# Optimization experiments

Measured on AMD Instinct MI355X. Metric: run time of the kernel, lower is better.

## Reference

```python
import jax, jax.numpy as jnp
import numpy as np
import math

B, C, D, NH, L, DFF = 128, 112, 512, 8, 13, 1920
DK = D // NH  # 64
_pos = np.arange(64)
_ranks, _files = _pos // 8, _pos % 8
RIDX = np.clip(_ranks[:, None] - _ranks[None, :], -7, 7) + 7  # [64,64] rel-rank bucket
FIDX = np.clip(_files[:, None] - _files[None, :], -7, 7) + 7  # [64,64] rel-file bucket
DIAG = _ranks + _files        # [64] in [0,14]
ADIAG = _ranks - _files + 7   # [64] in [0,14]


def _ln(x, g, b):
    m = jnp.mean(x, -1, keepdims=True)
    v = jnp.mean((x - m) ** 2, -1, keepdims=True)
    return (x - m) * jax.lax.rsqrt(v + 1e-5) * g + b


def setup_inputs() -> dict:
    key = jax.random.key(0)
    ks = iter(jax.random.split(key, 40))
    nrm = lambda *s: jax.random.normal(next(ks), s, jnp.float32) * 0.02
    return dict(
        x=jax.random.normal(next(ks), (B, C, 8, 8), jnp.float32),
        conv_w=nrm(C, D), conv_b=jnp.zeros(D),
        cls_token=nrm(1, 1, D),
        abs_pos=nrm(1, 64, D),
        file_emb=nrm(8, D), rank_emb=nrm(8, D),
        diag_emb=nrm(15, D), anti_diag_emb=nrm(15, D),
        ln1_g=jnp.ones((L, D)), ln1_b=jnp.zeros((L, D)),
        wq=nrm(L, D, D), bq=jnp.zeros((L, D)),
        wk=nrm(L, D, D), bk=jnp.zeros((L, D)),
        wv=nrm(L, D, D), bv=jnp.zeros((L, D)),
        wo=nrm(L, D, D), bo=jnp.zeros((L, D)),
        rel_bias=nrm(L, 15, 15, NH),
        ln2_g=jnp.ones((L, D)), ln2_b=jnp.zeros((L, D)),
        w_ff1=nrm(L, D, 2 * DFF), b_ff1=jnp.zeros((L, 2 * DFF)),
        w_ff2=nrm(L, DFF, D), b_ff2=jnp.zeros((L, D)),
        out_g=jnp.ones(D), out_b=jnp.zeros(D),
        vw1=nrm(D, D // 2), vb1=jnp.zeros(D // 2),
        vw2=nrm(D // 2, 128), vb2=jnp.zeros(128),
        vw3=nrm(128, 3), vb3=jnp.zeros(3),
        pw=nrm(D, 72), pb=jnp.zeros(72),
    )


def reference(x, conv_w, conv_b, cls_token, abs_pos, file_emb, rank_emb, diag_emb, anti_diag_emb,
              ln1_g, ln1_b, wq, bq, wk, bk, wv, bv, wo, bo, rel_bias, ln2_g, ln2_b,
              w_ff1, b_ff1, w_ff2, b_ff2, out_g, out_b,
              vw1, vb1, vw2, vb2, vw3, vb3, pw, pb):
    Bc = x.shape[0]
    # 1x1 conv == channel-wise linear; flatten spatial (row-major: s = rank*8 + file)
    tok = jnp.einsum('bcs,cd->bsd', x.reshape(Bc, C, 64), conv_w) + conv_b  # [B,64,D]
    pos = abs_pos + file_emb[_files] + rank_emb[_ranks] + diag_emb[DIAG] + anti_diag_emb[ADIAG]
    tok = tok + pos
    h = jnp.concatenate([jnp.broadcast_to(cls_token, (Bc, 1, D)), tok], axis=1)  # [B,65,D]
    scale = 1.0 / math.sqrt(DK)

    def block(hx, p):
        g1, b1, Wq, Bq, Wk, Bk, Wv, Bv, Wo, Bo, rb, g2, b2, W1, B1, W2, B2 = p
        n = _ln(hx, g1, b1)
        q = (n @ Wq + Bq).reshape(Bc, 65, NH, DK).transpose(0, 2, 1, 3)
        k = (n @ Wk + Bk).reshape(Bc, 65, NH, DK).transpose(0, 2, 1, 3)
        v = (n @ Wv + Bv).reshape(Bc, 65, NH, DK).transpose(0, 2, 1, 3)
        # gather relative-position bias [64,64,H] -> [H,65,65] with zero row/col for CLS
        bias = jnp.pad(jnp.transpose(rb[RIDX, FIDX], (2, 0, 1)), ((0, 0), (1, 0), (1, 0)))
        scores = jnp.einsum('bhqd,bhkd->bhqk', q, k) * scale + bias[None]
        a = jax.nn.softmax(scores, axis=-1)
        ctx = jnp.einsum('bhqk,bhkd->bhqd', a, v).transpose(0, 2, 1, 3).reshape(Bc, 65, D)
        hx = hx + ctx @ Wo + Bo
        n2 = _ln(hx, g2, b2)
        u = n2 @ W1 + B1
        u1, u2 = jnp.split(u, 2, axis=-1)
        hx = hx + (jax.nn.gelu(u1, approximate=False) * u2) @ W2 + B2
        return hx, None

    params = (ln1_g, ln1_b, wq, bq, wk, bk, wv, bv, wo, bo, rel_bias,
              ln2_g, ln2_b, w_ff1, b_ff1, w_ff2, b_ff2)
    h, _ = jax.lax.scan(block, h, params)
    h = _ln(h, out_g, out_b)
    cls = h[:, 0]
    v1 = jax.nn.gelu(cls @ vw1 + vb1, approximate=False)
    v2 = jax.nn.gelu(v1 @ vw2 + vb2, approximate=False)
    value = v2 @ vw3 + vb3                 # WDL logits [B,3]
    policy = (h[:, 1:] @ pw + pb).reshape(Bc, -1)  # [B, 64*72]
    return policy, value
```

## Files before the change

### kernel.cpp

```cpp
#include <hip/hip_runtime.h>
#include <stdint.h>

#define NLAYER 13
#define DMODEL 512
#define SEQ    65
#define BATCH  128
#define MROWS  (BATCH*SEQ)
#define NHEAD  8
#define DFFH   1920
#define MTILES 65
#define MBAND  9

typedef __bf16 bf16x8 __attribute__((ext_vector_type(8)));
typedef float  f32x4  __attribute__((ext_vector_type(4)));

__device__ __forceinline__ float bf2f(unsigned short u) {
    union { unsigned int i; float f; } c; c.i = ((unsigned int)u) << 16; return c.f;
}
__device__ __forceinline__ unsigned short f2bf(float f) {
    union { float f; unsigned int i; } c; c.f = f;
    unsigned int u = c.i;
    u += 0x7fffu + ((u >> 16) & 1u);
    return (unsigned short)(u >> 16);
}
__device__ __forceinline__ float gelu_exact(float x) {
    return 0.5f * x * (1.0f + erff(x * 0.70710678118654752f));
}

__global__ __launch_bounds__(256) void transpose_f32_bf16(
    const float* __restrict__ src, unsigned short* __restrict__ dst,
    int R, int C, int Cpad, long srcLS, long dstLS, int rowOff)
{
    __shared__ float tile[32][33];
    int l  = blockIdx.z;
    int c0 = blockIdx.x * 32, r0 = blockIdx.y * 32;
    const float* s = src + (long)l * srcLS;
    unsigned short* d = dst + (long)l * dstLS;
    int tx = threadIdx.x, ty = threadIdx.y;
#pragma unroll
    for (int k = 0; k < 4; k++) {
        int r = r0 + ty + 8*k, c = c0 + tx;
        float v = (r < R && c < C) ? s[(long)r * C + c] : 0.0f;
        tile[ty + 8*k][tx] = v;
    }
    __syncthreads();
#pragma unroll
    for (int k = 0; k < 4; k++) {
        int c = c0 + ty + 8*k, r = r0 + tx;
        if (c < Cpad && r < R)
            d[(long)(rowOff + c) * R + r] = f2bf(tile[tx][ty + 8*k]);
    }
}

__global__ __launch_bounds__(256) void stack_bias_kernel(
    const float* __restrict__ bq, const float* __restrict__ bk,
    const float* __restrict__ bv, float* __restrict__ bqkv)
{
    int idx = blockIdx.x * 256 + threadIdx.x;
    if (idx >= NLAYER * 1536) return;
    int l = idx / 1536, r = idx - l * 1536;
    float v;
    if (r < 512)       v = bq[l*512 + r];
    else if (r < 1024) v = bk[l*512 + r - 512];
    else               v = bv[l*512 + r - 1024];
    bqkv[idx] = v;
}

__global__ __launch_bounds__(256) void embed_kernel(
    const float* __restrict__ x, const float* __restrict__ conv_w,
    const float* __restrict__ conv_b, const float* __restrict__ cls_tok,
    const float* __restrict__ abs_pos, const float* __restrict__ file_emb,
    const float* __restrict__ rank_emb, const float* __restrict__ diag_emb,
    const float* __restrict__ adiag_emb, float* __restrict__ h)
{
    int b = blockIdx.y, sg = blockIdx.x, t = threadIdx.x;
    if (sg == 8) {
        for (int d = t; d < 512; d += 256)
            h[(long)b * SEQ * 512 + d] = cls_tok[d];
        return;
    }
    __shared__ float xs[112][8];
    for (int idx = t; idx < 112*8; idx += 256) {
        int c = idx >> 3, j = idx & 7;
        xs[c][j] = x[((long)b*112 + c)*64 + sg*8 + j];
    }
    __syncthreads();
    int d0 = t, d1 = t + 256;
    float acc0[8] = {}, acc1[8] = {};
    for (int c = 0; c < 112; c++) {
        float w0 = conv_w[c*512 + d0], w1 = conv_w[c*512 + d1];
#pragma unroll
        for (int j = 0; j < 8; j++) { acc0[j] += xs[c][j]*w0; acc1[j] += xs[c][j]*w1; }
    }
#pragma unroll
    for (int j = 0; j < 8; j++) {
        int sq = sg*8 + j, r = sq >> 3, f = sq & 7;
        long row = ((long)b * SEQ + 1 + sq) * 512;
        h[row + d0] = acc0[j] + conv_b[d0] + abs_pos[sq*512+d0] + file_emb[f*512+d0]
                    + rank_emb[r*512+d0] + diag_emb[(r+f)*512+d0] + adiag_emb[(r-f+7)*512+d0];
        h[row + d1] = acc1[j] + conv_b[d1] + abs_pos[sq*512+d1] + file_emb[f*512+d1]
                    + rank_emb[r*512+d1] + diag_emb[(r+f)*512+d1] + adiag_emb[(r-f+7)*512+d1];
    }
}

__global__ __launch_bounds__(256) void ln_kernel(
    const float* __restrict__ hx, const float* __restrict__ g,
    const float* __restrict__ bb, unsigned short* __restrict__ o)
{
    int row  = blockIdx.x * 4 + (threadIdx.x >> 6);
    int lane = threadIdx.x & 63;
    const float4* xr = (const float4*)(hx + (long)row * 512);
    float4 v0 = xr[lane], v1 = xr[lane + 64];
    float s  = v0.x+v0.y+v0.z+v0.w + v1.x+v1.y+v1.z+v1.w;
    float s2 = v0.x*v0.x+v0.y*v0.y+v0.z*v0.z+v0.w*v0.w
             + v1.x*v1.x+v1.y*v1.y+v1.z*v1.z+v1.w*v1.w;
    for (int off = 32; off; off >>= 1) { s += __shfl_xor(s, off); s2 += __shfl_xor(s2, off); }
    float mean = s * (1.0f/512.0f);
    float var  = s2 * (1.0f/512.0f) - mean*mean;
    float rs   = rsqrtf(var + 1e-5f);
    const float4* gr = (const float4*)g; const float4* br = (const float4*)bb;
    float4 g0 = gr[lane], g1 = gr[lane+64], b0 = br[lane], b1 = br[lane+64];
    ushort4 o0, o1;
    o0.x = f2bf((v0.x-mean)*rs*g0.x + b0.x);
    o0.y = f2bf((v0.y-mean)*rs*g0.y + b0.y);
    o0.z = f2bf((v0.z-mean)*rs*g0.z + b0.z);
    o0.w = f2bf((v0.w-mean)*rs*g0.w + b0.w);
    o1.x = f2bf((v1.x-mean)*rs*g1.x + b1.x);
    o1.y = f2bf((v1.y-mean)*rs*g1.y + b1.y);
    o1.z = f2bf((v1.z-mean)*rs*g1.z + b1.z);
    o1.w = f2bf((v1.w-mean)*rs*g1.w + b1.w);
    ushort4* orow = (ushort4*)(o + (long)row * 512);
    orow[lane] = o0; orow[lane + 64] = o1;
}

template<int MODE>
__global__ __launch_bounds__(256) void gemm128(
    const unsigned short* __restrict__ A, const unsigned short* __restrict__ Bt,
    const float* __restrict__ bias, const float* __restrict__ res,
    void* __restrict__ out, int K, int ldo, int nT)
{
    __shared__ __attribute__((aligned(16))) unsigned short As[128*32];
    __shared__ __attribute__((aligned(16))) unsigned short Bs[128*32];
    int id = blockIdx.x;
    int xcd = id & 7, jj = id >> 3;
    int bn  = jj % nT;
    int mt  = xcd * MBAND + jj / nT;
    if (mt >= MTILES) return;
    int m0 = mt * 128;
    int tid = threadIdx.x;
    int lane = tid & 63, w = tid >> 6;
    int quad = lane >> 4, col = lane & 15;

    int srow = tid >> 2;
    int sc8  = (tid & 3) * 8;

    int br0, br1;
    if (MODE == 2) {
        br0 = bn*64 + srow;
        br1 = 1920 + bn*64 + srow;
    } else {
        br0 = bn*128 + srow;
        br1 = bn*128 + srow + 64;
    }
    const unsigned short* Arow0 = A + (long)(m0 + srow) * K + sc8;
    const unsigned short* Arow1 = A + (long)(m0 + srow + 64) * K + sc8;
    const unsigned short* Brow0 = Bt + (long)br0 * K + sc8;
    const unsigned short* Brow1 = Bt + (long)br1 * K + sc8;

    f32x4 acc[2][8] = {};

    int4 ca0 = *(const int4*)(Arow0);
    int4 ca1 = *(const int4*)(Arow1);
    int4 cb0 = *(const int4*)(Brow0);
    int4 cb1 = *(const int4*)(Brow1);

    for (int k0 = 0; k0 < K; k0 += 32) {
        __syncthreads();
        *(int4*)(&As[srow*32 + sc8])        = ca0;
        *(int4*)(&As[(srow+64)*32 + sc8])   = ca1;
        *(int4*)(&Bs[srow*32 + sc8])        = cb0;
        *(int4*)(&Bs[(srow+64)*32 + sc8])   = cb1;
        __syncthreads();
        int kn = k0 + 32;
        if (kn < K) {
            ca0 = *(const int4*)(Arow0 + kn);
            ca1 = *(const int4*)(Arow1 + kn);
            cb0 = *(const int4*)(Brow0 + kn);
            cb1 = *(const int4*)(Brow1 + kn);
        }
        bf16x8 af[2], bfr[8];
#pragma unroll
        for (int i = 0; i < 2; i++)
            af[i] = *(const bf16x8*)(&As[(w*32 + i*16 + col)*32 + quad*8]);
#pragma unroll
        for (int t = 0; t < 8; t++)
            bfr[t] = *(const bf16x8*)(&Bs[(t*16 + col)*32 + quad*8]);
#pragma unroll
        for (int i = 0; i < 2; i++)
#pragma unroll
            for (int t = 0; t < 8; t++)
                acc[i][t] = __builtin_amdgcn_mfma_f32_16x16x32_bf16(af[i], bfr[t], acc[i][t], 0, 0, 0);
    }

    if (MODE == 2) {
        unsigned short* O = (unsigned short*)out;
        int gn0 = bn * 64;
#pragma unroll
        for (int i = 0; i < 2; i++)
#pragma unroll
        for (int t = 0; t < 4; t++) {
            int c = t*16 + col;
            float b1v = bias[gn0 + c];
            float b2v = bias[1920 + gn0 + c];
#pragma unroll
            for (int r = 0; r < 4; r++) {
                int m = m0 + w*32 + i*16 + quad*4 + r;
                float u1 = acc[i][t][r]   + b1v;
                float u2 = acc[i][t+4][r] + b2v;
                O[(long)m * DFFH + gn0 + c] = f2bf(gelu_exact(u1) * u2);
            }
        }
        return;
    }
    int n0 = bn * 128;
#pragma unroll
    for (int i = 0; i < 2; i++)
#pragma unroll
    for (int t = 0; t < 8; t++) {
        int cg = n0 + t*16 + col;
        float bv = (MODE == 3) ? (cg < 72 ? bias[cg] : 0.0f) : bias[cg];
#pragma unroll
        for (int r = 0; r < 4; r++) {
            int m = m0 + w*32 + i*16 + quad*4 + r;
            float v = acc[i][t][r] + bv;
            if (MODE == 0) {
                ((unsigned short*)out)[(long)m * ldo + cg] = f2bf(v);
            } else if (MODE == 1) {
                ((float*)out)[(long)m * ldo + cg] = res[(long)m * ldo + cg] + v;
            } else {
                if (cg < 72) {
                    int b2 = m / 65, s = m - b2 * 65;
                    if (s > 0)
                        ((float*)out)[(long)b2 * 4608 + (s - 1) * 72 + cg] = v;
                }
            }
        }
    }
}

__global__ __launch_bounds__(256) void attn_mfma_kernel(
    const unsigned short* __restrict__ qkv,
    const float* __restrict__ rel_bias,
    unsigned short* __restrict__ ctx,
    int layer)
{
    constexpr int QS = 72;
    constexpr int VS = 104;
    constexpr int SS = 68;
    constexpr int PS = 104;
    __shared__ __attribute__((aligned(16))) unsigned short Qs[80*QS];
    __shared__ __attribute__((aligned(16))) unsigned short Ks[80*QS];
    __shared__ __attribute__((aligned(16))) unsigned short Vt[64*VS];
    __shared__ __attribute__((aligned(16))) float Sf[65*SS];
    __shared__ __attribute__((aligned(16))) unsigned short Pb[80*PS];
    __shared__ float bias_s[225];

    int h = blockIdx.x, b = blockIdx.y, t = threadIdx.x;
    int lane = t & 63, w = t >> 6;
    int quad = lane >> 4, col = lane & 15;

    for (int i = t; i < 225; i += 256)
        bias_s[i] = rel_bias[((long)layer*225 + i)*8 + h];

    for (int i = t; i < 65*8; i += 256) {
        int s = i >> 3, c8 = (i & 7) * 8;
        const unsigned short* row = qkv + ((long)(b*65+s))*1536 + h*64 + c8;
        int4 qv = *(const int4*)(row);
        int4 kv = *(const int4*)(row + 512);
        int4 vv = *(const int4*)(row + 1024);
        unsigned short qsc[8];
        const unsigned short* qp = (const unsigned short*)&qv;
#pragma unroll
        for (int j = 0; j < 8; j++) qsc[j] = f2bf(bf2f(qp[j]) * 0.125f);
        *(int4*)&Qs[s*QS + c8] = *(const int4*)qsc;
        *(int4*)&Ks[s*QS + c8] = kv;
        const unsigned short* vp = (const unsigned short*)&vv;
#pragma unroll
        for (int j = 0; j < 8; j++) Vt[(c8+j)*VS + s] = vp[j];
    }
    for (int i = t; i < 64*31; i += 256) {
        int d = i / 31, s = 65 + i % 31;
        Vt[d*VS + s] = 0;
    }
    __syncthreads();

    for (int tt = w; tt < 25; tt += 4) {
        int mi = tt / 5, nj = tt % 5;
        f32x4 acc = {};
        bf16x8 a0 = *(const bf16x8*)&Qs[(mi*16+col)*QS + quad*8];
        bf16x8 b0 = *(const bf16x8*)&Ks[(nj*16+col)*QS + quad*8];
        acc = __builtin_amdgcn_mfma_f32_16x16x32_bf16(a0, b0, acc, 0, 0, 0);
        bf16x8 a1 = *(const bf16x8*)&Qs[(mi*16+col)*QS + 32 + quad*8];
        bf16x8 b1 = *(const bf16x8*)&Ks[(nj*16+col)*QS + 32 + quad*8];
        acc = __builtin_amdgcn_mfma_f32_16x16x32_bf16(a1, b1, acc, 0, 0, 0);
#pragma unroll
        for (int r = 0; r < 4; r++) {
            int qi = mi*16 + quad*4 + r, kj = nj*16 + col;
            if (qi < 65 && kj < 65) {
                float v = acc[r];
                if (qi >= 1 && kj >= 1) {
                    int i2 = qi - 1, j2 = kj - 1;
                    int dr = (i2 >> 3) - (j2 >> 3) + 7;
                    int df = (i2 & 7) - (j2 & 7) + 7;
                    v += bias_s[dr*15 + df];
                }
                Sf[qi*SS + kj] = v;
            }
        }
    }
    __syncthreads();

    for (int r = w; r < 65; r += 4) {
        float x0 = Sf[r*SS + lane];
        float x1 = (lane == 0) ? Sf[r*SS + 64] : -1e30f;
        float mx = fmaxf(x0, x1);
        for (int off = 32; off; off >>= 1) mx = fmaxf(mx, __shfl_xor(mx, off));
        float e0 = __expf(x0 - mx);
        float e1 = (lane == 0) ? __expf(x1 - mx) : 0.0f;
        float sm = e0 + e1;
        for (int off = 32; off; off >>= 1) sm += __shfl_xor(sm, off);
        float inv = 1.0f / sm;
        Pb[r*PS + lane] = f2bf(e0 * inv);
        if (lane == 0)  Pb[r*PS + 64] = f2bf(e1 * inv);
        if (lane >= 1 && lane <= 31) Pb[r*PS + 64 + lane] = 0;
    }
    __syncthreads();

    for (int tt = w; tt < 20; tt += 4) {
        int mi = tt >> 2, dj = tt & 3;
        f32x4 acc = {};
#pragma unroll
        for (int ks = 0; ks < 3; ks++) {
            bf16x8 a  = *(const bf16x8*)&Pb[(mi*16+col)*PS + ks*32 + quad*8];
            bf16x8 bb = *(const bf16x8*)&Vt[(dj*16+col)*VS + ks*32 + quad*8];
            acc = __builtin_amdgcn_mfma_f32_16x16x32_bf16(a, bb, acc, 0, 0, 0);
        }
#pragma unroll
        for (int r = 0; r < 4; r++) {
            int qi = mi*16 + quad*4 + r;
            if (qi < 65)
                ctx[((long)(b*65+qi))*512 + h*64 + dj*16 + col] = f2bf(acc[r]);
        }
    }
}

__global__ __launch_bounds__(256) void value_head_kernel(
    const unsigned short* __restrict__ hn,
    const float* __restrict__ vw1, const float* __restrict__ vb1,
    const float* __restrict__ vw2, const float* __restrict__ vb2,
    const float* __restrict__ vw3, const float* __restrict__ vb3,
    float* __restrict__ outv)
{
    int b = blockIdx.x, t = threadIdx.x;
    __shared__ float cls[512], v1[256], v2[128];
    for (int d = t; d < 512; d += 256) cls[d] = bf2f(hn[(long)b * SEQ * 512 + d]);
    __syncthreads();
    {
        float a = vb1[t];
        for (int c = 0; c < 512; c++) a += cls[c] * vw1[c*256 + t];
        v1[t] = gelu_exact(a);
    }
    __syncthreads();
    if (t < 128) {
        float a = vb2[t];
        for (int c = 0; c < 256; c++) a += v1[c] * vw2[c*128 + t];
        v2[t] = gelu_exact(a);
    }
    __syncthreads();
    if (t < 3) {
        float a = vb3[t];
        for (int c = 0; c < 128; c++) a += v2[c] * vw3[c*3 + t];
        outv[b*3 + t] = a;
    }
}

extern "C" void kernel_launch(void* const* d_in, const int* in_sizes, int n_in,
                              void* d_out, int out_size, void* d_ws, size_t ws_size,
                              hipStream_t stream)
{
    (void)in_sizes; (void)n_in; (void)out_size; (void)ws_size;
    const float* x        = (const float*)d_in[0];
    const float* conv_w   = (const float*)d_in[1];
    const float* conv_b   = (const float*)d_in[2];
    const float* cls_tok  = (const float*)d_in[3];
    const float* abs_pos  = (const float*)d_in[4];
    const float* file_emb = (const float*)d_in[5];
    const float* rank_emb = (const float*)d_in[6];
    const float* diag_emb = (const float*)d_in[7];
    const float* adiag    = (const float*)d_in[8];
    const float* ln1_g    = (const float*)d_in[9];
    const float* ln1_b    = (const float*)d_in[10];
    const float* wq       = (const float*)d_in[11];
    const float* bq       = (const float*)d_in[12];
    const float* wk       = (const float*)d_in[13];
    const float* bk       = (const float*)d_in[14];
    const float* wv       = (const float*)d_in[15];
    const float* bv       = (const float*)d_in[16];
    const float* wo       = (const float*)d_in[17];
    const float* bo       = (const float*)d_in[18];
    const float* rel_bias = (const float*)d_in[19];
    const float* ln2_g    = (const float*)d_in[20];
    const float* ln2_b    = (const float*)d_in[21];
    const float* w_ff1    = (const float*)d_in[22];
    const float* b_ff1    = (const float*)d_in[23];
    const float* w_ff2    = (const float*)d_in[24];
    const float* b_ff2    = (const float*)d_in[25];
    const float* out_g    = (const float*)d_in[26];
    const float* out_b    = (const float*)d_in[27];
    const float* vw1      = (const float*)d_in[28];
    const float* vb1      = (const float*)d_in[29];
    const float* vw2      = (const float*)d_in[30];
    const float* vb2      = (const float*)d_in[31];
    const float* vw3      = (const float*)d_in[32];
    const float* vb3      = (const float*)d_in[33];
    const float* pw       = (const float*)d_in[34];
    const float* pb       = (const float*)d_in[35];

    char* p = (char*)d_ws;
    auto alloc = [&](size_t bytes) { void* r = (void*)p; p += (bytes + 255) & ~(size_t)255; return r; };
    unsigned short* qkvT = (unsigned short*)alloc((size_t)NLAYER*1536*512*2);
    unsigned short* woT  = (unsigned short*)alloc((size_t)NLAYER*512*512*2);
    unsigned short* w1T  = (unsigned short*)alloc((size_t)NLAYER*3840*512*2);
    unsigned short* w2T  = (unsigned short*)alloc((size_t)NLAYER*512*1920*2);
    unsigned short* pwT  = (unsigned short*)alloc((size_t)128*512*2);
    float*          bqkv = (float*)alloc((size_t)NLAYER*1536*4);
    float*          h    = (float*)alloc((size_t)MROWS*512*4);
    unsigned short* nbf  = (unsigned short*)alloc((size_t)MROWS*512*2);
    unsigned short* qkvb = (unsigned short*)alloc((size_t)MROWS*1536*2);
    unsigned short* ctxb = (unsigned short*)alloc((size_t)MROWS*512*2);
    unsigned short* gbuf = (unsigned short*)alloc((size_t)MROWS*1920*2);

    dim3 tb(32, 8);
    transpose_f32_bf16<<<dim3(16,16,NLAYER), tb, 0, stream>>>(wq, qkvT, 512, 512, 512, 512L*512, 1536L*512, 0);
    transpose_f32_bf16<<<dim3(16,16,NLAYER), tb, 0, stream>>>(wk, qkvT, 512, 512, 512, 512L*512, 1536L*512, 512);
    transpose_f32_bf16<<<dim3(16,16,NLAYER), tb, 0, stream>>>(wv, qkvT, 512, 512, 512, 512L*512, 1536L*512, 1024);
    transpose_f32_bf16<<<dim3(16,16,NLAYER), tb, 0, stream>>>(wo, woT, 512, 512, 512, 512L*512, 512L*512, 0);
    transpose_f32_bf16<<<dim3(120,16,NLAYER), tb, 0, stream>>>(w_ff1, w1T, 512, 3840, 3840, 512L*3840, 3840L*512, 0);
    transpose_f32_bf16<<<dim3(16,60,NLAYER), tb, 0, stream>>>(w_ff2, w2T, 1920, 512, 512, 1920L*512, 512L*1920, 0);
    transpose_f32_bf16<<<dim3(4,16,1), tb, 0, stream>>>(pw, pwT, 512, 72, 128, 0, 0, 0);
    stack_bias_kernel<<<(NLAYER*1536 + 255)/256, 256, 0, stream>>>(bq, bk, bv, bqkv);

    embed_kernel<<<dim3(9, BATCH), 256, 0, stream>>>(x, conv_w, conv_b, cls_tok, abs_pos,
                                                     file_emb, rank_emb, diag_emb, adiag, h);

    for (int l = 0; l < NLAYER; l++) {
        ln_kernel<<<MROWS/4, 256, 0, stream>>>(h, ln1_g + l*512, ln1_b + l*512, nbf);
        gemm128<0><<<72*12, 256, 0, stream>>>(nbf, qkvT + (size_t)l*1536*512,
                                              bqkv + l*1536, nullptr, qkvb, 512, 1536, 12);
        attn_mfma_kernel<<<dim3(NHEAD, BATCH), 256, 0, stream>>>(qkvb, rel_bias, ctxb, l);
        gemm128<1><<<72*4, 256, 0, stream>>>(ctxb, woT + (size_t)l*512*512,
                                             bo + l*512, h, h, 512, 512, 4);
        ln_kernel<<<MROWS/4, 256, 0, stream>>>(h, ln2_g + l*512, ln2_b + l*512, nbf);
        gemm128<2><<<72*30, 256, 0, stream>>>(nbf, w1T + (size_t)l*3840*512,
                                              b_ff1 + l*3840, nullptr, gbuf, 512, 0, 30);
        gemm128<1><<<72*4, 256, 0, stream>>>(gbuf, w2T + (size_t)l*512*1920,
                                             b_ff2 + l*512, h, h, 1920, 512, 4);
    }

    ln_kernel<<<MROWS/4, 256, 0, stream>>>(h, out_g, out_b, nbf);
    gemm128<3><<<72*1, 256, 0, stream>>>(nbf, pwT, pb, nullptr, (float*)d_out, 512, 0, 1);
    value_head_kernel<<<BATCH, 256, 0, stream>>>(nbf, vw1, vb1, vw2, vb2, vw3, vb3,
                                                 (float*)d_out + (size_t)BATCH*4608);
}
```

Measured before the change: 2.908 ms.

## Double-buffer LDS tiles in gemm128 to drop one barrier per k-step

The GEMM main loop now uses two LDS buffers for the A and B tiles. The next tile is stored to the alternate buffer while MFMAs run on the current one, and the global load for the tile after that is issued early. This removes one of the two __syncthreads per 32-wide k-step and overlaps LDS writes with compute. In exchange LDS use doubles to 32KB per block, which may lower occupancy, and the unrolled loop assumes K is a multiple of 64.

```diff
diff --git a/kernel.cpp b/kernel.cpp
--- a/kernel.cpp
+++ b/kernel.cpp
@@ -139,8 +139,8 @@
     const float* __restrict__ bias, const float* __restrict__ res,
     void* __restrict__ out, int K, int ldo, int nT)
 {
-    __shared__ __attribute__((aligned(16))) unsigned short As[128*32];
-    __shared__ __attribute__((aligned(16))) unsigned short Bs[128*32];
+    __shared__ __attribute__((aligned(16))) unsigned short As[2*128*32];
+    __shared__ __attribute__((aligned(16))) unsigned short Bs[2*128*32];
     int id = blockIdx.x;
     int xcd = id & 7, jj = id >> 3;
     int bn  = jj % nT;
@@ -173,34 +173,50 @@
     int4 ca1 = *(const int4*)(Arow1);
     int4 cb0 = *(const int4*)(Brow0);
     int4 cb1 = *(const int4*)(Brow1);
-
-    for (int k0 = 0; k0 < K; k0 += 32) {
-        __syncthreads();
-        *(int4*)(&As[srow*32 + sc8])        = ca0;
-        *(int4*)(&As[(srow+64)*32 + sc8])   = ca1;
-        *(int4*)(&Bs[srow*32 + sc8])        = cb0;
-        *(int4*)(&Bs[(srow+64)*32 + sc8])   = cb1;
-        __syncthreads();
-        int kn = k0 + 32;
-        if (kn < K) {
-            ca0 = *(const int4*)(Arow0 + kn);
-            ca1 = *(const int4*)(Arow1 + kn);
-            cb0 = *(const int4*)(Brow0 + kn);
-            cb1 = *(const int4*)(Brow1 + kn);
-        }
-        bf16x8 af[2], bfr[8];
-#pragma unroll
-        for (int i = 0; i < 2; i++)
-            af[i] = *(const bf16x8*)(&As[(w*32 + i*16 + col)*32 + quad*8]);
-#pragma unroll
-        for (int t = 0; t < 8; t++)
-            bfr[t] = *(const bf16x8*)(&Bs[(t*16 + col)*32 + quad*8]);
-#pragma unroll
-        for (int i = 0; i < 2; i++)
-#pragma unroll
-            for (int t = 0; t < 8; t++)
-                acc[i][t] = __builtin_amdgcn_mfma_f32_16x16x32_bf16(af[i], bfr[t], acc[i][t], 0, 0, 0);
-    }
+    *(int4*)(&As[srow*32 + sc8])        = ca0;
+    *(int4*)(&As[(srow+64)*32 + sc8])   = ca1;
+    *(int4*)(&Bs[srow*32 + sc8])        = cb0;
+    *(int4*)(&Bs[(srow+64)*32 + sc8])   = cb1;
+    ca0 = *(const int4*)(Arow0 + 32);
+    ca1 = *(const int4*)(Arow1 + 32);
+    cb0 = *(const int4*)(Brow0 + 32);
+    cb1 = *(const int4*)(Brow1 + 32);
+    __syncthreads();
+
+#define GSTEP(BUFC, BUFN, kt)                                                  \
+    {                                                                          \
+        bf16x8 af[2], bfr[8];                                                  \
+        _Pragma("unroll")                                                      \
+        for (int i = 0; i < 2; i++)                                            \
+            af[i] = *(const bf16x8*)(&As[(BUFC) + (w*32 + i*16 + col)*32 + quad*8]); \
+        _Pragma("unroll")                                                      \
+        for (int t = 0; t < 8; t++)                                            \
+            bfr[t] = *(const bf16x8*)(&Bs[(BUFC) + (t*16 + col)*32 + quad*8]); \
+        if ((kt) + 32 < K) {                                                   \
+            *(int4*)(&As[(BUFN) + srow*32 + sc8])      = ca0;                  \
+            *(int4*)(&As[(BUFN) + (srow+64)*32 + sc8]) = ca1;                  \
+            *(int4*)(&Bs[(BUFN) + srow*32 + sc8])      = cb0;                  \
+            *(int4*)(&Bs[(BUFN) + (srow+64)*32 + sc8]) = cb1;                  \
+            if ((kt) + 64 < K) {                                               \
+                ca0 = *(const int4*)(Arow0 + (kt) + 64);                       \
+                ca1 = *(const int4*)(Arow1 + (kt) + 64);                       \
+                cb0 = *(const int4*)(Brow0 + (kt) + 64);                       \
+                cb1 = *(const int4*)(Brow1 + (kt) + 64);                       \
+            }                                                                  \
+        }                                                                      \
+        _Pragma("unroll")                                                      \
+        for (int i = 0; i < 2; i++)                                            \
+        _Pragma("unroll")                                                      \
+            for (int t = 0; t < 8; t++)                                        \
+                acc[i][t] = __builtin_amdgcn_mfma_f32_16x16x32_bf16(af[i], bfr[t], acc[i][t], 0, 0, 0); \
+        __syncthreads();                                                       \
+    }
+
+    for (int k0 = 0; k0 < K; k0 += 64) {
+        GSTEP(0,    4096, k0);
+        GSTEP(4096, 0,    k0 + 32);
+    }
+#undef GSTEP
 
     if (MODE == 2) {
         unsigned short* O = (unsigned short*)out;
```

New measurement: 2.833 ms. 2.6% less time.
